# Kernel optimization log

Measured on AMD Instinct MI355X. Metric: run time of the kernel, lower is better.

The kernel has to match this reference:

```python
import jax, jax.numpy as jnp
import numpy as np
import math

B, T, C, H, DFF = 4, 2048, 1024, 16, 4096
HD = C // H
EPS = 1e-5


def _layernorm(x, g, b):
    mu = jnp.mean(x, axis=-1, keepdims=True)
    var = jnp.var(x, axis=-1, keepdims=True)
    return (x - mu) * jax.lax.rsqrt(var + EPS) * g + b


def _new_gelu(x):
    # 0.5*x*(1+tanh(sqrt(2/pi)*(x+0.044715*x^3)))
    c = math.sqrt(2.0 / math.pi)
    return 0.5 * x * (1.0 + jnp.tanh(c * (x + 0.044715 * x ** 3)))


def setup_inputs() -> dict:
    key = jax.random.key(0)
    ks = jax.random.split(key, 12)
    s = lambda fan_in: 1.0 / math.sqrt(fan_in)
    return {
        "x": jax.random.normal(ks[0], (B, T, C), jnp.float32),
        "ln1_g": jnp.ones((C,), jnp.float32),
        "ln1_b": jnp.zeros((C,), jnp.float32),
        "w_qkv": jax.random.normal(ks[1], (C, 3 * C), jnp.float32) * s(C),
        "b_qkv": jnp.zeros((3 * C,), jnp.float32),
        "w_o": jax.random.normal(ks[2], (C, C), jnp.float32) * s(C),
        "b_o": jnp.zeros((C,), jnp.float32),
        "ln2_g": jnp.ones((C,), jnp.float32),
        "ln2_b": jnp.zeros((C,), jnp.float32),
        "w_fc": jax.random.normal(ks[3], (C, DFF), jnp.float32) * s(C),
        "b_fc": jnp.zeros((DFF,), jnp.float32),
        "w_proj": jax.random.normal(ks[4], (DFF, C), jnp.float32) * s(DFF),
        "b_proj": jnp.zeros((C,), jnp.float32),
    }


def reference(x, ln1_g, ln1_b, w_qkv, b_qkv, w_o, b_o, ln2_g, ln2_b, w_fc, b_fc, w_proj, b_proj):
    # --- attention sub-block ---
    h = _layernorm(x, ln1_g, ln1_b)
    qkv = h @ w_qkv + b_qkv                                  # (B,T,3C)
    q, k, v = jnp.split(qkv, 3, axis=-1)
    q = q.reshape(B, T, H, HD).transpose(0, 2, 1, 3)          # (B,H,T,hd)
    k = k.reshape(B, T, H, HD).transpose(0, 2, 1, 3)
    v = v.reshape(B, T, H, HD).transpose(0, 2, 1, 3)
    scores = jnp.einsum("bhqd,bhkd->bhqk", q, k) / math.sqrt(HD)
    causal = jnp.tril(jnp.ones((T, T), jnp.bool_))            # (T,T)
    scores = jnp.where(causal[None, None], scores, -jnp.inf)
    probs = jax.nn.softmax(scores, axis=-1)
    attn = jnp.einsum("bhqk,bhkd->bhqd", probs, v)
    attn = attn.transpose(0, 2, 1, 3).reshape(B, T, C)
    x = x + attn @ w_o + b_o
    # --- MLP sub-block ---
    h2 = _layernorm(x, ln2_g, ln2_b)
    x = x + _new_gelu(h2 @ w_fc + b_fc) @ w_proj + b_proj
    return x
```

## Files before the change

### kernel.cpp

```cpp
#include <hip/hip_runtime.h>
#include <hip/hip_bf16.h>

using bf16 = __hip_bfloat16;
typedef __attribute__((ext_vector_type(8))) short bf16x8;
typedef __attribute__((ext_vector_type(4))) float f32x4;
typedef __attribute__((ext_vector_type(16))) float f32x16;

#define LOG2E 1.4426950408889634f

__device__ inline short f2b(float f) {
  __hip_bfloat16 h = __float2bfloat16(f);
  return *reinterpret_cast<short*>(&h);
}
__device__ inline float b2f(short s) {
  unsigned int u = ((unsigned int)(unsigned short)s) << 16;
  float f;
  __builtin_memcpy(&f, &u, 4);
  return f;
}
__device__ inline unsigned pk2(float a, float b) {
  return (unsigned)(unsigned short)f2b(a) |
         ((unsigned)(unsigned short)f2b(b) << 16);
}

__global__ __launch_bounds__(256) void transpose_cast_kernel(
    const float* __restrict__ in, bf16* __restrict__ out, int K, int N) {
  __shared__ float tile[32][33];
  int tx = threadIdx.x & 31;
  int ty = threadIdx.x >> 5;
  int n0 = blockIdx.x * 32, k0 = blockIdx.y * 32;
#pragma unroll
  for (int i = 0; i < 4; i++)
    tile[ty + i * 8][tx] = in[(size_t)(k0 + ty + i * 8) * N + n0 + tx];
  __syncthreads();
#pragma unroll
  for (int i = 0; i < 4; i++)
    out[(size_t)(n0 + ty + i * 8) * K + k0 + tx] =
        __float2bfloat16(tile[tx][ty + i * 8]);
}

__global__ __launch_bounds__(256) void transpose_v_kernel(
    const bf16* __restrict__ qkv, bf16* __restrict__ vt) {
  __shared__ short tile[64][66];
  const int bh = blockIdx.y;
  const int b = bh >> 4, h = bh & 15;
  const int t0 = blockIdx.x * 64;
  const int tid = threadIdx.x;
  const int r = tid >> 3, c8 = (tid & 7) * 8;
#pragma unroll
  for (int p = 0; p < 2; p++) {
    int t = r + p * 32;
    bf16x8 v = *(const bf16x8*)&qkv[(size_t)(b * 2048 + t0 + t) * 3072 + 2048 +
                                    h * 64 + c8];
#pragma unroll
    for (int i = 0; i < 8; i++) tile[t][c8 + i] = v[i];
  }
  __syncthreads();
#pragma unroll
  for (int p = 0; p < 2; p++) {
    int d = r + p * 32;
    int tt = c8;
    bf16x8 o;
#pragma unroll
    for (int i = 0; i < 8; i++) o[i] = tile[tt + i][d];
    *(bf16x8*)&vt[(size_t)(bh * 64 + d) * 2048 + t0 + tt] = o;
  }
}

__global__ __launch_bounds__(256) void ln_kernel(
    const float* __restrict__ x, const float* __restrict__ g,
    const float* __restrict__ b, bf16* __restrict__ out) {
  int row = blockIdx.x;
  const float4 v = ((const float4*)(x + (size_t)row * 1024))[threadIdx.x];
  float s = v.x + v.y + v.z + v.w;
  float ss = v.x * v.x + v.y * v.y + v.z * v.z + v.w * v.w;
#pragma unroll
  for (int off = 1; off < 64; off <<= 1) {
    s += __shfl_xor(s, off);
    ss += __shfl_xor(ss, off);
  }
  __shared__ float red[2][4];
  int w = threadIdx.x >> 6, lane = threadIdx.x & 63;
  if (lane == 0) { red[0][w] = s; red[1][w] = ss; }
  __syncthreads();
  s = red[0][0] + red[0][1] + red[0][2] + red[0][3];
  ss = red[1][0] + red[1][1] + red[1][2] + red[1][3];
  float mu = s * (1.0f / 1024.0f);
  float var = ss * (1.0f / 1024.0f) - mu * mu;
  float rstd = rsqrtf(var + 1e-5f);
  const float4 gv = ((const float4*)g)[threadIdx.x];
  const float4 bv = ((const float4*)b)[threadIdx.x];
  short4 o4;
  o4.x = f2b((v.x - mu) * rstd * gv.x + bv.x);
  o4.y = f2b((v.y - mu) * rstd * gv.y + bv.y);
  o4.z = f2b((v.z - mu) * rstd * gv.z + bv.z);
  o4.w = f2b((v.w - mu) * rstd * gv.w + bv.w);
  ((short4*)out)[(size_t)row * 256 + threadIdx.x] = o4;
}

__global__ __launch_bounds__(256) void fused_ln_kernel(
    const float* __restrict__ p0, const float* __restrict__ p1,
    const float* __restrict__ bo, const float* __restrict__ x,
    const float* __restrict__ g, const float* __restrict__ bln,
    float* __restrict__ x1, bf16* __restrict__ h2) {
  int row = blockIdx.x;
  size_t base = (size_t)row * 256 + threadIdx.x;
  float4 a = ((const float4*)p0)[base];
  float4 c = ((const float4*)p1)[base];
  float4 xr = ((const float4*)x)[base];
  float4 bo4 = ((const float4*)bo)[threadIdx.x];
  float4 v;
  v.x = a.x + c.x + xr.x + bo4.x;
  v.y = a.y + c.y + xr.y + bo4.y;
  v.z = a.z + c.z + xr.z + bo4.z;
  v.w = a.w + c.w + xr.w + bo4.w;
  ((float4*)x1)[base] = v;
  float s = v.x + v.y + v.z + v.w;
  float ss = v.x * v.x + v.y * v.y + v.z * v.z + v.w * v.w;
#pragma unroll
  for (int off = 1; off < 64; off <<= 1) {
    s += __shfl_xor(s, off);
    ss += __shfl_xor(ss, off);
  }
  __shared__ float red[2][4];
  int w = threadIdx.x >> 6, lane = threadIdx.x & 63;
  if (lane == 0) { red[0][w] = s; red[1][w] = ss; }
  __syncthreads();
  s = red[0][0] + red[0][1] + red[0][2] + red[0][3];
  ss = red[1][0] + red[1][1] + red[1][2] + red[1][3];
  float mu = s * (1.0f / 1024.0f);
  float var = ss * (1.0f / 1024.0f) - mu * mu;
  float rstd = rsqrtf(var + 1e-5f);
  const float4 gv = ((const float4*)g)[threadIdx.x];
  const float4 bv = ((const float4*)bln)[threadIdx.x];
  short4 o4;
  o4.x = f2b((v.x - mu) * rstd * gv.x + bv.x);
  o4.y = f2b((v.y - mu) * rstd * gv.y + bv.y);
  o4.z = f2b((v.z - mu) * rstd * gv.z + bv.z);
  o4.w = f2b((v.w - mu) * rstd * gv.w + bv.w);
  ((short4*)h2)[base] = o4;
}

__global__ __launch_bounds__(256) void fused_add_kernel(
    float* __restrict__ out, const float* __restrict__ q1,
    const float* __restrict__ x1, const float* __restrict__ bp, int n4) {
  for (int i = blockIdx.x * 256 + threadIdx.x; i < n4; i += gridDim.x * 256) {
    float4 a = ((const float4*)out)[i];
    float4 c = ((const float4*)q1)[i];
    float4 xr = ((const float4*)x1)[i];
    float4 b4 = ((const float4*)bp)[i & 255];
    float4 v;
    v.x = a.x + c.x + xr.x + b4.x;
    v.y = a.y + c.y + xr.y + b4.y;
    v.z = a.z + c.z + xr.z + b4.z;
    v.w = a.w + c.w + xr.w + b4.w;
    ((float4*)out)[i] = v;
  }
}

template <int EPI>
__global__ __launch_bounds__(512, 1) void gemm256_kernel(
    const bf16* __restrict__ A, const bf16* __restrict__ Bt,
    const float* __restrict__ bias, float* __restrict__ out0,
    float* __restrict__ out1, void* __restrict__ outv, int M, int N, int Kfull,
    int Ksub, int ntiles) {
  __shared__ short As[2][256 * 64];
  __shared__ short Bs[2][256 * 64];
  const int tid = threadIdx.x;
  const int lane = tid & 63, wid = tid >> 6;
  const int wr = wid >> 2, wc = wid & 3;

  const int nwg = gridDim.x;
  const int flat = blockIdx.x;
  const int sw = (flat & 7) * (nwg >> 3) + (flat >> 3);
  const int kq = sw / ntiles;
  const int tile = sw % ntiles;
  const int gy = M >> 8;
  const int bcol = tile / gy, brow = tile % gy;
  const int koff = kq * Ksub;
  const int nk = Ksub >> 6;

  const int srow = tid >> 3;
  const int schs = (tid & 7) ^ (srow & 7);

  const bf16* gA[4];
  const bf16* gB[4];
  int dstL[4];
#pragma unroll
  for (int r = 0; r < 4; r++) {
    gA[r] = A + (size_t)(brow * 256 + r * 64 + srow) * Kfull + koff + schs * 8;
    gB[r] = Bt + (size_t)(bcol * 256 + r * 64 + srow) * Kfull + koff + schs * 8;
    dstL[r] = (r * 64 + wid * 8) * 64;
  }

  auto stA_half = [&](int kt, int buf, int hf) {
#pragma unroll
    for (int rr = 0; rr < 2; rr++) {
      const int r = hf * 2 + rr;
      __builtin_amdgcn_global_load_lds(
          (const __attribute__((address_space(1))) unsigned int*)(gA[r] +
                                                                  kt * 64),
          (__attribute__((address_space(3))) unsigned int*)&As[buf][dstL[r]],
          16, 0, 0);
    }
  };
  auto stB_half = [&](int kt, int buf, int hf) {
#pragma unroll
    for (int rr = 0; rr < 2; rr++) {
      const int r = hf * 2 + rr;
      __builtin_amdgcn_global_load_lds(
          (const __attribute__((address_space(1))) unsigned int*)(gB[r] +
                                                                  kt * 64),
          (__attribute__((address_space(3))) unsigned int*)&Bs[buf][dstL[r]],
          16, 0, 0);
    }
  };

  int ofA[2][4][2], ofB[2][2][2];
#pragma unroll
  for (int qm = 0; qm < 2; qm++)
#pragma unroll
    for (int mm = 0; mm < 4; mm++)
#pragma unroll
      for (int ks = 0; ks < 2; ks++) {
        int row = wr * 128 + qm * 64 + mm * 16 + (lane & 15);
        int ch = (ks * 4 + (lane >> 4)) ^ (row & 7);
        ofA[qm][mm][ks] = row * 64 + ch * 8;
      }
#pragma unroll
  for (int qn = 0; qn < 2; qn++)
#pragma unroll
    for (int nn = 0; nn < 2; nn++)
#pragma unroll
      for (int ks = 0; ks < 2; ks++) {
        int row = wc * 64 + qn * 32 + nn * 16 + (lane & 15);
        int ch = (ks * 4 + (lane >> 4)) ^ (row & 7);
        ofB[qn][nn][ks] = row * 64 + ch * 8;
      }

  f32x4 acc[8][4] = {};
  bf16x8 af[4][2], bf0[2][2], bf1[2][2];

  stA_half(0, 0, 0);
  stA_half(0, 0, 1);
  stB_half(0, 0, 0);
  stB_half(0, 0, 1);
  if (nk > 1) {
    stB_half(1, 1, 0);
    stB_half(1, 1, 1);
    asm volatile("s_waitcnt vmcnt(4)" ::: "memory");
  } else {
    asm volatile("s_waitcnt vmcnt(0)" ::: "memory");
  }
  __builtin_amdgcn_s_barrier();

  for (int t = 0; t < nk; t++) {
    const int cur = t & 1, nxt = cur ^ 1;
    const short* Ac = As[cur];
    const short* Bc = Bs[cur];
#pragma unroll
    for (int mm = 0; mm < 4; mm++)
#pragma unroll
      for (int ks = 0; ks < 2; ks++)
        af[mm][ks] = *(const bf16x8*)&Ac[ofA[0][mm][ks]];
#pragma unroll
    for (int nn = 0; nn < 2; nn++)
#pragma unroll
      for (int ks = 0; ks < 2; ks++)
        bf0[nn][ks] = *(const bf16x8*)&Bc[ofB[0][nn][ks]];
    if (t + 1 < nk) stA_half(t + 1, nxt, 0);
    __builtin_amdgcn_s_barrier();
    asm volatile("s_waitcnt lgkmcnt(0)" ::: "memory");
    __builtin_amdgcn_sched_barrier(0);
    __builtin_amdgcn_s_setprio(1);
#pragma unroll
    for (int mm = 0; mm < 4; mm++)
#pragma unroll
      for (int nn = 0; nn < 2; nn++)
#pragma unroll
        for (int ks = 0; ks < 2; ks++)
          acc[mm][nn] = __builtin_amdgcn_mfma_f32_16x16x32_bf16(
              af[mm][ks], bf0[nn][ks], acc[mm][nn], 0, 0, 0);
    __builtin_amdgcn_s_setprio(0);
    __builtin_amdgcn_s_barrier();
#pragma unroll
    for (int nn = 0; nn < 2; nn++)
#pragma unroll
      for (int ks = 0; ks < 2; ks++)
        bf1[nn][ks] = *(const bf16x8*)&Bc[ofB[1][nn][ks]];
    if (t + 1 < nk) stA_half(t + 1, nxt, 1);
    __builtin_amdgcn_s_barrier();
    asm volatile("s_waitcnt lgkmcnt(0)" ::: "memory");
    __builtin_amdgcn_sched_barrier(0);
    __builtin_amdgcn_s_setprio(1);
#pragma unroll
    for (int mm = 0; mm < 4; mm++)
#pragma unroll
      for (int nn = 0; nn < 2; nn++)
#pragma unroll
        for (int ks = 0; ks < 2; ks++)
          acc[mm][2 + nn] = __builtin_amdgcn_mfma_f32_16x16x32_bf16(
              af[mm][ks], bf1[nn][ks], acc[mm][2 + nn], 0, 0, 0);
    __builtin_amdgcn_s_setprio(0);
    __builtin_amdgcn_s_barrier();
#pragma unroll
    for (int mm = 0; mm < 4; mm++)
#pragma unroll
      for (int ks = 0; ks < 2; ks++)
        af[mm][ks] = *(const bf16x8*)&Ac[ofA[1][mm][ks]];
    if (t + 2 < nk) stB_half(t + 2, cur, 0);
    __builtin_amdgcn_s_barrier();
    asm volatile("s_waitcnt lgkmcnt(0)" ::: "memory");
    __builtin_amdgcn_sched_barrier(0);
    __builtin_amdgcn_s_setprio(1);
#pragma unroll
    for (int mm = 0; mm < 4; mm++)
#pragma unroll
      for (int nn = 0; nn < 2; nn++)
#pragma unroll
        for (int ks = 0; ks < 2; ks++)
          acc[4 + mm][2 + nn] = __builtin_amdgcn_mfma_f32_16x16x32_bf16(
              af[mm][ks], bf1[nn][ks], acc[4 + mm][2 + nn], 0, 0, 0);
    __builtin_amdgcn_s_setprio(0);
    __builtin_amdgcn_s_barrier();
    if (t + 2 < nk) stB_half(t + 2, cur, 1);
    __builtin_amdgcn_s_setprio(1);
#pragma unroll
    for (int mm = 0; mm < 4; mm++)
#pragma unroll
      for (int nn = 0; nn < 2; nn++)
#pragma unroll
        for (int ks = 0; ks < 2; ks++)
          acc[4 + mm][nn] = __builtin_amdgcn_mfma_f32_16x16x32_bf16(
              af[mm][ks], bf0[nn][ks], acc[4 + mm][nn], 0, 0, 0);
    __builtin_amdgcn_s_setprio(0);
    if (t + 2 < nk)
      asm volatile("s_waitcnt vmcnt(4)" ::: "memory");
    else if (t + 1 < nk)
      asm volatile("s_waitcnt vmcnt(0)" ::: "memory");
    __builtin_amdgcn_s_barrier();
  }

#pragma unroll
  for (int m = 0; m < 8; m++)
#pragma unroll
    for (int n = 0; n < 4; n++) {
      int gr0 = brow * 256 + wr * 128 + m * 16 + (lane >> 4) * 4;
      int gc = bcol * 256 + wc * 64 + n * 16 + (lane & 15);
      if constexpr (EPI == 3) {
        float* po = kq ? out1 : out0;
#pragma unroll
        for (int j = 0; j < 4; j++)
          po[(size_t)(gr0 + j) * N + gc] = acc[m][n][j];
      } else {
        float bia = bias[gc];
#pragma unroll
        for (int j = 0; j < 4; j++) {
          float v = acc[m][n][j] + bia;
          size_t idx = (size_t)(gr0 + j) * N + gc;
          if constexpr (EPI == 0) {
            ((bf16*)outv)[idx] = __float2bfloat16(v);
          } else {
            float u = 0.7978845608028654f * (v + 0.044715f * v * v * v);
            float t2 = exp2f(u * (2.0f * LOG2E));
            float th = 1.0f - 2.0f / (t2 + 1.0f);
            ((bf16*)outv)[idx] = __float2bfloat16(0.5f * v * (1.0f + th));
          }
        }
      }
    }
}

__global__ __launch_bounds__(256) void attn_kernel(
    const bf16* __restrict__ qkv, const bf16* __restrict__ vt,
    bf16* __restrict__ attn) {
  const int bh = blockIdx.x;
  const int qt = 15 - blockIdx.y;
  const int b = bh >> 4, h = bh & 15;
  const int tid = threadIdx.x, w = tid >> 6, lane = tid & 63;
  const int col = lane & 31;
  const int hi = lane >> 5;

  __shared__ short Kl[2][64 * 64];
  __shared__ short Vl[2][64 * 64];

  const int qbase = qt * 128 + w * 32;
  const int qglob = qbase + col;
  const size_t qrow = (size_t)(b * 2048 + qglob);

  bf16x8 qf[4];
#pragma unroll
  for (int dks = 0; dks < 4; dks++) {
    bf16x8 raw =
        *(const bf16x8*)&qkv[qrow * 3072 + h * 64 + dks * 16 + hi * 8];
#pragma unroll
    for (int i = 0; i < 8; i++) qf[dks][i] = f2b(b2f(raw[i]) * 0.125f);
  }

  auto stage = [&](int kt, int buf) {
    const int kv0s = kt * 64;
#pragma unroll
    for (int j = 0; j < 2; j++) {
      int c = (j * 4 + w) * 64 + lane;
      int row = c >> 3;
      int sw8 = ((c & 7) ^ (row & 7)) * 8;
      const bf16* gk =
          qkv + (size_t)(b * 2048 + kv0s + row) * 3072 + 1024 + h * 64 + sw8;
      __builtin_amdgcn_global_load_lds(
          (const __attribute__((address_space(1))) unsigned int*)gk,
          (__attribute__((address_space(3))) unsigned int*)(
              &Kl[buf][(j * 4 + w) * 512]),
          16, 0, 0);
      const bf16* gv = vt + (size_t)(bh * 64 + row) * 2048 + kv0s + sw8;
      __builtin_amdgcn_global_load_lds(
          (const __attribute__((address_space(1))) unsigned int*)gv,
          (__attribute__((address_space(3))) unsigned int*)(
              &Vl[buf][(j * 4 + w) * 512]),
          16, 0, 0);
    }
  };

  f32x16 ot[2] = {};
  float m = -1e30f, l = 0.0f;

  const int ktend = qt * 2 + 1;
  stage(0, 0);
  for (int kt = 0; kt <= ktend; kt++) {
    const int kv0 = kt * 64;
    const int cur = kt & 1;
    if (kt < ktend) {
      stage(kt + 1, cur ^ 1);
      asm volatile("s_waitcnt vmcnt(4)" ::: "memory");
    } else {
      asm volatile("s_waitcnt vmcnt(0)" ::: "memory");
    }
    __builtin_amdgcn_s_barrier();

    if (kv0 <= qbase + 31) {
      f32x16 st[2] = {};
#pragma unroll
      for (int s = 0; s < 2; s++) {
        int kvrow = s * 32 + col;
        int swz = kvrow & 7;
#pragma unroll
        for (int dks = 0; dks < 4; dks++) {
          int ch = (dks * 2 + hi) ^ swz;
          bf16x8 kf = *(const bf16x8*)&Kl[cur][kvrow * 64 + ch * 8];
          st[s] = __builtin_amdgcn_mfma_f32_32x32x16_bf16(kf, qf[dks], st[s],
                                                          0, 0, 0);
        }
      }
      if (kv0 + 63 > qbase) {
#pragma unroll
        for (int s = 0; s < 2; s++)
#pragma unroll
          for (int r = 0; r < 16; r++) {
            int kv = kv0 + s * 32 + (r & 3) + 8 * (r >> 2) + 4 * hi;
            if (kv > qglob) st[s][r] = -1e30f;
          }
      }
      float vm[16];
#pragma unroll
      for (int i = 0; i < 16; i++) vm[i] = fmaxf(st[0][i], st[1][i]);
#pragma unroll
      for (int w2 = 8; w2 >= 1; w2 >>= 1)
#pragma unroll
        for (int i = 0; i < w2; i++) vm[i] = fmaxf(vm[i], vm[i + w2]);
      float pmax = fmaxf(vm[0], __shfl_xor(vm[0], 32));
      if (!__all(pmax - m <= 8.0f)) {
        float mnew = fmaxf(m, pmax);
        float corr = exp2f((m - mnew) * LOG2E);
        m = mnew;
        l *= corr;
#pragma unroll
        for (int s = 0; s < 2; s++)
#pragma unroll
          for (int r = 0; r < 16; r++) ot[s][r] *= corr;
      }
#pragma unroll
      for (int s = 0; s < 2; s++)
#pragma unroll
        for (int r = 0; r < 16; r++)
          st[s][r] = exp2f((st[s][r] - m) * LOG2E);
      float vs[16];
#pragma unroll
      for (int i = 0; i < 16; i++) vs[i] = st[0][i] + st[1][i];
#pragma unroll
      for (int w2 = 8; w2 >= 1; w2 >>= 1)
#pragma unroll
        for (int i = 0; i < w2; i++) vs[i] += vs[i + w2];
      l += vs[0] + __shfl_xor(vs[0], 32);

#pragma unroll
      for (int sub = 0; sub < 2; sub++) {
#pragma unroll
        for (int kl = 0; kl < 2; kl++) {
          unsigned A0 = pk2(st[sub][kl * 8 + 0], st[sub][kl * 8 + 1]);
          unsigned A1 = pk2(st[sub][kl * 8 + 2], st[sub][kl * 8 + 3]);
          unsigned B0 = pk2(st[sub][kl * 8 + 4], st[sub][kl * 8 + 5]);
          unsigned B1 = pk2(st[sub][kl * 8 + 6], st[sub][kl * 8 + 7]);
          unsigned sA0 = (unsigned)__shfl_xor((int)A0, 32);
          unsigned sA1 = (unsigned)__shfl_xor((int)A1, 32);
          unsigned sB0 = (unsigned)__shfl_xor((int)B0, 32);
          unsigned sB1 = (unsigned)__shfl_xor((int)B1, 32);
          union { unsigned u[4]; bf16x8 v; } pf;
          pf.u[0] = hi ? sB0 : A0;
          pf.u[1] = hi ? sB1 : A1;
          pf.u[2] = hi ? B0 : sA0;
          pf.u[3] = hi ? B1 : sA1;
          int ks = sub * 2 + kl;
#pragma unroll
          for (int ds = 0; ds < 2; ds++) {
            int drow = ds * 32 + col;
            int ch = (ks * 2 + hi) ^ (drow & 7);
            bf16x8 vf = *(const bf16x8*)&Vl[cur][drow * 64 + ch * 8];
            ot[ds] = __builtin_amdgcn_mfma_f32_32x32x16_bf16(vf, pf.v, ot[ds],
                                                             0, 0, 0);
          }
        }
      }
    }
    __builtin_amdgcn_s_barrier();
  }

  float rl = 1.0f / l;
#pragma unroll
  for (int ds = 0; ds < 2; ds++)
#pragma unroll
    for (int j = 0; j < 4; j++) {
      ushort4 o4;
      o4.x = (unsigned short)f2b(ot[ds][4 * j + 0] * rl);
      o4.y = (unsigned short)f2b(ot[ds][4 * j + 1] * rl);
      o4.z = (unsigned short)f2b(ot[ds][4 * j + 2] * rl);
      o4.w = (unsigned short)f2b(ot[ds][4 * j + 3] * rl);
      *(ushort4*)&attn[qrow * 1024 + h * 64 + 32 * ds + 8 * j + 4 * hi] = o4;
    }
}

extern "C" void kernel_launch(void* const* d_in, const int* in_sizes, int n_in,
                              void* d_out, int out_size, void* d_ws,
                              size_t ws_size, hipStream_t stream) {
  (void)in_sizes; (void)n_in; (void)out_size; (void)ws_size;
  const float* x      = (const float*)d_in[0];
  const float* ln1_g  = (const float*)d_in[1];
  const float* ln1_b  = (const float*)d_in[2];
  const float* w_qkv  = (const float*)d_in[3];
  const float* b_qkv  = (const float*)d_in[4];
  const float* w_o    = (const float*)d_in[5];
  const float* b_o    = (const float*)d_in[6];
  const float* ln2_g  = (const float*)d_in[7];
  const float* ln2_b  = (const float*)d_in[8];
  const float* w_fc   = (const float*)d_in[9];
  const float* b_fc   = (const float*)d_in[10];
  const float* w_proj = (const float*)d_in[11];
  const float* b_proj = (const float*)d_in[12];
  float* out = (float*)d_out;

  char* ws = (char*)d_ws;
  const size_t MB = 1048576;
  float* x1     = (float*)(ws + 0);
  bf16* slotA   = (bf16*)(ws + 32 * MB);
  bf16* wt_qkv  = (bf16*)(ws + 48 * MB);
  bf16* wt_o    = (bf16*)(ws + 54 * MB);
  bf16* wt_fc   = (bf16*)(ws + 56 * MB);
  bf16* wt_proj = (bf16*)(ws + 64 * MB);
  bf16* qkvb    = (bf16*)(ws + 72 * MB);
  bf16* vtb     = (bf16*)(ws + 120 * MB);
  float* p0     = (float*)(ws + 72 * MB);
  float* p1     = (float*)(ws + 104 * MB);
  bf16* gbuf    = (bf16*)(ws + 72 * MB);
  float* q1     = (float*)(ws + 32 * MB);

  dim3 blk(256);
  transpose_cast_kernel<<<dim3(3072 / 32, 1024 / 32), blk, 0, stream>>>(
      w_qkv, wt_qkv, 1024, 3072);
  transpose_cast_kernel<<<dim3(1024 / 32, 1024 / 32), blk, 0, stream>>>(
      w_o, wt_o, 1024, 1024);
  transpose_cast_kernel<<<dim3(4096 / 32, 1024 / 32), blk, 0, stream>>>(
      w_fc, wt_fc, 1024, 4096);
  transpose_cast_kernel<<<dim3(1024 / 32, 4096 / 32), blk, 0, stream>>>(
      w_proj, wt_proj, 4096, 1024);

  ln_kernel<<<8192, blk, 0, stream>>>(x, ln1_g, ln1_b, slotA);
  gemm256_kernel<0><<<dim3(384), dim3(512), 0, stream>>>(
      slotA, wt_qkv, b_qkv, nullptr, nullptr, qkvb, 8192, 3072, 1024, 1024,
      384);
  transpose_v_kernel<<<dim3(32, 64), blk, 0, stream>>>(qkvb, vtb);
  attn_kernel<<<dim3(64, 16), blk, 0, stream>>>(qkvb, vtb, slotA);
  gemm256_kernel<3><<<dim3(256), dim3(512), 0, stream>>>(
      slotA, wt_o, nullptr, p0, p1, nullptr, 8192, 1024, 1024, 512, 128);
  fused_ln_kernel<<<8192, blk, 0, stream>>>(p0, p1, b_o, x, ln2_g, ln2_b, x1,
                                            slotA);
  gemm256_kernel<2><<<dim3(512), dim3(512), 0, stream>>>(
      slotA, wt_fc, b_fc, nullptr, nullptr, gbuf, 8192, 4096, 1024, 1024, 512);
  gemm256_kernel<3><<<dim3(256), dim3(512), 0, stream>>>(
      gbuf, wt_proj, nullptr, out, q1, nullptr, 8192, 1024, 4096, 2048, 128);
  fused_add_kernel<<<dim3(2048), blk, 0, stream>>>(out, q1, x1, b_proj,
                                                   2097152);
}
```

Measured before the change: 424.1 us.

## Run attention as single-wave blocks reading K/V straight from global memory

The attention kernel becomes one 64-thread wave per 32-query band, with 4096 blocks instead of 1024. The double-buffered LDS staging and block barriers are removed, and each wave loads its K and V fragments directly from global memory into registers for the MFMAs. This drops barrier synchronisation and the idle waves in causal blocks, and gives finer-grained causal load balance. In exchange, K/V tiles are no longer shared across four waves through LDS, so global/L2 traffic rises, and direct loads are no longer prefetched ahead of use.

```diff
diff --git a/kernel.cpp b/kernel.cpp
--- a/kernel.cpp
+++ b/kernel.cpp
@@ -371,20 +371,17 @@
     }
 }
 
-__global__ __launch_bounds__(256) void attn_kernel(
+__global__ __launch_bounds__(64) void attn_kernel(
     const bf16* __restrict__ qkv, const bf16* __restrict__ vt,
     bf16* __restrict__ attn) {
   const int bh = blockIdx.x;
-  const int qt = 15 - blockIdx.y;
+  const int band = 63 - blockIdx.y;
   const int b = bh >> 4, h = bh & 15;
-  const int tid = threadIdx.x, w = tid >> 6, lane = tid & 63;
+  const int lane = threadIdx.x;
   const int col = lane & 31;
   const int hi = lane >> 5;
 
-  __shared__ short Kl[2][64 * 64];
-  __shared__ short Vl[2][64 * 64];
-
-  const int qbase = qt * 128 + w * 32;
+  const int qbase = band * 32;
   const int qglob = qbase + col;
   const size_t qrow = (size_t)(b * 2048 + qglob);
 
@@ -397,130 +394,94 @@
     for (int i = 0; i < 8; i++) qf[dks][i] = f2b(b2f(raw[i]) * 0.125f);
   }
 
-  auto stage = [&](int kt, int buf) {
-    const int kv0s = kt * 64;
-#pragma unroll
-    for (int j = 0; j < 2; j++) {
-      int c = (j * 4 + w) * 64 + lane;
-      int row = c >> 3;
-      int sw8 = ((c & 7) ^ (row & 7)) * 8;
-      const bf16* gk =
-          qkv + (size_t)(b * 2048 + kv0s + row) * 3072 + 1024 + h * 64 + sw8;
-      __builtin_amdgcn_global_load_lds(
-          (const __attribute__((address_space(1))) unsigned int*)gk,
-          (__attribute__((address_space(3))) unsigned int*)(
-              &Kl[buf][(j * 4 + w) * 512]),
-          16, 0, 0);
-      const bf16* gv = vt + (size_t)(bh * 64 + row) * 2048 + kv0s + sw8;
-      __builtin_amdgcn_global_load_lds(
-          (const __attribute__((address_space(1))) unsigned int*)gv,
-          (__attribute__((address_space(3))) unsigned int*)(
-              &Vl[buf][(j * 4 + w) * 512]),
-          16, 0, 0);
-    }
-  };
+  const bf16* Kbase = qkv + (size_t)(b * 2048) * 3072 + 1024 + h * 64;
+  const bf16* Vbase = vt + (size_t)(bh * 64) * 2048;
 
   f32x16 ot[2] = {};
   float m = -1e30f, l = 0.0f;
 
-  const int ktend = qt * 2 + 1;
-  stage(0, 0);
+  const int ktend = (qbase + 31) >> 6;
   for (int kt = 0; kt <= ktend; kt++) {
     const int kv0 = kt * 64;
-    const int cur = kt & 1;
-    if (kt < ktend) {
-      stage(kt + 1, cur ^ 1);
-      asm volatile("s_waitcnt vmcnt(4)" ::: "memory");
-    } else {
-      asm volatile("s_waitcnt vmcnt(0)" ::: "memory");
-    }
-    __builtin_amdgcn_s_barrier();
-
-    if (kv0 <= qbase + 31) {
-      f32x16 st[2] = {};
-#pragma unroll
-      for (int s = 0; s < 2; s++) {
-        int kvrow = s * 32 + col;
-        int swz = kvrow & 7;
-#pragma unroll
-        for (int dks = 0; dks < 4; dks++) {
-          int ch = (dks * 2 + hi) ^ swz;
-          bf16x8 kf = *(const bf16x8*)&Kl[cur][kvrow * 64 + ch * 8];
-          st[s] = __builtin_amdgcn_mfma_f32_32x32x16_bf16(kf, qf[dks], st[s],
-                                                          0, 0, 0);
+    f32x16 st[2] = {};
+#pragma unroll
+    for (int s = 0; s < 2; s++) {
+      const bf16* krow = Kbase + (size_t)(kv0 + s * 32 + col) * 3072 + hi * 8;
+#pragma unroll
+      for (int dks = 0; dks < 4; dks++) {
+        bf16x8 kf = *(const bf16x8*)(krow + dks * 16);
+        st[s] = __builtin_amdgcn_mfma_f32_32x32x16_bf16(kf, qf[dks], st[s],
+                                                        0, 0, 0);
+      }
+    }
+    if (kv0 + 63 > qbase) {
+#pragma unroll
+      for (int s = 0; s < 2; s++)
+#pragma unroll
+        for (int r = 0; r < 16; r++) {
+          int kv = kv0 + s * 32 + (r & 3) + 8 * (r >> 2) + 4 * hi;
+          if (kv > qglob) st[s][r] = -1e30f;
+        }
+    }
+    float vm[16];
+#pragma unroll
+    for (int i = 0; i < 16; i++) vm[i] = fmaxf(st[0][i], st[1][i]);
+#pragma unroll
+    for (int w2 = 8; w2 >= 1; w2 >>= 1)
+#pragma unroll
+      for (int i = 0; i < w2; i++) vm[i] = fmaxf(vm[i], vm[i + w2]);
+    float pmax = fmaxf(vm[0], __shfl_xor(vm[0], 32));
+    if (!__all(pmax - m <= 8.0f)) {
+      float mnew = fmaxf(m, pmax);
+      float corr = exp2f((m - mnew) * LOG2E);
+      m = mnew;
+      l *= corr;
+#pragma unroll
+      for (int s = 0; s < 2; s++)
+#pragma unroll
+        for (int r = 0; r < 16; r++) ot[s][r] *= corr;
+    }
+#pragma unroll
+    for (int s = 0; s < 2; s++)
+#pragma unroll
+      for (int r = 0; r < 16; r++) st[s][r] = exp2f((st[s][r] - m) * LOG2E);
+    float vs[16];
+#pragma unroll
+    for (int i = 0; i < 16; i++) vs[i] = st[0][i] + st[1][i];
+#pragma unroll
+    for (int w2 = 8; w2 >= 1; w2 >>= 1)
+#pragma unroll
+      for (int i = 0; i < w2; i++) vs[i] += vs[i + w2];
+    l += vs[0] + __shfl_xor(vs[0], 32);
+
+#pragma unroll
+    for (int sub = 0; sub < 2; sub++) {
+#pragma unroll
+      for (int kl = 0; kl < 2; kl++) {
+        unsigned A0 = pk2(st[sub][kl * 8 + 0], st[sub][kl * 8 + 1]);
+        unsigned A1 = pk2(st[sub][kl * 8 + 2], st[sub][kl * 8 + 3]);
+        unsigned B0 = pk2(st[sub][kl * 8 + 4], st[sub][kl * 8 + 5]);
+        unsigned B1 = pk2(st[sub][kl * 8 + 6], st[sub][kl * 8 + 7]);
+        unsigned sA0 = (unsigned)__shfl_xor((int)A0, 32);
+        unsigned sA1 = (unsigned)__shfl_xor((int)A1, 32);
+        unsigned sB0 = (unsigned)__shfl_xor((int)B0, 32);
+        unsigned sB1 = (unsigned)__shfl_xor((int)B1, 32);
+        union { unsigned u[4]; bf16x8 v; } pf;
+        pf.u[0] = hi ? sB0 : A0;
+        pf.u[1] = hi ? sB1 : A1;
+        pf.u[2] = hi ? B0 : sA0;
+        pf.u[3] = hi ? B1 : sA1;
+        int ks = sub * 2 + kl;
+#pragma unroll
+        for (int ds = 0; ds < 2; ds++) {
+          const bf16* vrow = Vbase + (size_t)(ds * 32 + col) * 2048 + kv0 +
+                             ks * 16 + hi * 8;
+          bf16x8 vf = *(const bf16x8*)vrow;
+          ot[ds] = __builtin_amdgcn_mfma_f32_32x32x16_bf16(vf, pf.v, ot[ds],
+                                                           0, 0, 0);
         }
       }
-      if (kv0 + 63 > qbase) {
-#pragma unroll
-        for (int s = 0; s < 2; s++)
-#pragma unroll
-          for (int r = 0; r < 16; r++) {
-            int kv = kv0 + s * 32 + (r & 3) + 8 * (r >> 2) + 4 * hi;
-            if (kv > qglob) st[s][r] = -1e30f;
-          }
-      }
-      float vm[16];
-#pragma unroll
-      for (int i = 0; i < 16; i++) vm[i] = fmaxf(st[0][i], st[1][i]);
-#pragma unroll
-      for (int w2 = 8; w2 >= 1; w2 >>= 1)
-#pragma unroll
-        for (int i = 0; i < w2; i++) vm[i] = fmaxf(vm[i], vm[i + w2]);
-      float pmax = fmaxf(vm[0], __shfl_xor(vm[0], 32));
-      if (!__all(pmax - m <= 8.0f)) {
-        float mnew = fmaxf(m, pmax);
-        float corr = exp2f((m - mnew) * LOG2E);
-        m = mnew;
-        l *= corr;
-#pragma unroll
-        for (int s = 0; s < 2; s++)
-#pragma unroll
-          for (int r = 0; r < 16; r++) ot[s][r] *= corr;
-      }
-#pragma unroll
-      for (int s = 0; s < 2; s++)
-#pragma unroll
-        for (int r = 0; r < 16; r++)
-          st[s][r] = exp2f((st[s][r] - m) * LOG2E);
-      float vs[16];
-#pragma unroll
-      for (int i = 0; i < 16; i++) vs[i] = st[0][i] + st[1][i];
-#pragma unroll
-      for (int w2 = 8; w2 >= 1; w2 >>= 1)
-#pragma unroll
-        for (int i = 0; i < w2; i++) vs[i] += vs[i + w2];
-      l += vs[0] + __shfl_xor(vs[0], 32);
-
-#pragma unroll
-      for (int sub = 0; sub < 2; sub++) {
-#pragma unroll
-        for (int kl = 0; kl < 2; kl++) {
-          unsigned A0 = pk2(st[sub][kl * 8 + 0], st[sub][kl * 8 + 1]);
-          unsigned A1 = pk2(st[sub][kl * 8 + 2], st[sub][kl * 8 + 3]);
-          unsigned B0 = pk2(st[sub][kl * 8 + 4], st[sub][kl * 8 + 5]);
-          unsigned B1 = pk2(st[sub][kl * 8 + 6], st[sub][kl * 8 + 7]);
-          unsigned sA0 = (unsigned)__shfl_xor((int)A0, 32);
-          unsigned sA1 = (unsigned)__shfl_xor((int)A1, 32);
-          unsigned sB0 = (unsigned)__shfl_xor((int)B0, 32);
-          unsigned sB1 = (unsigned)__shfl_xor((int)B1, 32);
-          union { unsigned u[4]; bf16x8 v; } pf;
-          pf.u[0] = hi ? sB0 : A0;
-          pf.u[1] = hi ? sB1 : A1;
-          pf.u[2] = hi ? B0 : sA0;
-          pf.u[3] = hi ? B1 : sA1;
-          int ks = sub * 2 + kl;
-#pragma unroll
-          for (int ds = 0; ds < 2; ds++) {
-            int drow = ds * 32 + col;
-            int ch = (ks * 2 + hi) ^ (drow & 7);
-            bf16x8 vf = *(const bf16x8*)&Vl[cur][drow * 64 + ch * 8];
-            ot[ds] = __builtin_amdgcn_mfma_f32_32x32x16_bf16(vf, pf.v, ot[ds],
-                                                             0, 0, 0);
-          }
-        }
-      }
-    }
-    __builtin_amdgcn_s_barrier();
+    }
   }
 
   float rl = 1.0f / l;
@@ -586,7 +547,7 @@
       slotA, wt_qkv, b_qkv, nullptr, nullptr, qkvb, 8192, 3072, 1024, 1024,
       384);
   transpose_v_kernel<<<dim3(32, 64), blk, 0, stream>>>(qkvb, vtb);
-  attn_kernel<<<dim3(64, 16), blk, 0, stream>>>(qkvb, vtb, slotA);
+  attn_kernel<<<dim3(64, 64), dim3(64), 0, stream>>>(qkvb, vtb, slotA);
   gemm256_kernel<3><<<dim3(256), dim3(512), 0, stream>>>(
       slotA, wt_o, nullptr, p0, p1, nullptr, 8192, 1024, 1024, 512, 128);
   fused_ln_kernel<<<8192, blk, 0, stream>>>(p0, p1, b_o, x, ln2_g, ln2_b, x1,
```

Result: slower. 467.9 us (+10.3%).
